# Optimization experiments

Hardware: AMD Instinct MI355X
Metric: run time of the kernel (lower is better)

The kernel has to match this reference:

```python
import jax, jax.numpy as jnp
import numpy as np

DIM = 1024   # model dim
H = 16       # query heads
KV = 2       # kv heads (GQA)
D = DIM // H # head_dim = 64
W = 256      # window_size
HW = W // 2  # half window = 128


def setup_inputs() -> dict:
    key = jax.random.key(0)
    ks = jax.random.split(key, 9)
    B, S = 2, 4096
    n = lambda k, shp, sc=1.0: jax.random.normal(k, shp, jnp.float32) * sc
    return {
        "x": n(ks[0], (B, S, DIM)),
        "Wq": n(ks[1], (DIM, H * D), 0.02), "bq": n(ks[2], (H * D,), 0.02),
        "Wk": n(ks[3], (DIM, KV * D), 0.02), "bk": n(ks[4], (KV * D,), 0.02),
        "Wv": n(ks[5], (DIM, KV * D), 0.02), "bv": n(ks[6], (KV * D,), 0.02),
        "Wo": n(ks[7], (DIM, DIM), 0.02), "bo": n(ks[8], (DIM,), 0.02),
    }


def reference(x, Wq, bq, Wk, bk, Wv, bv, Wo, bo):
    B, S, _ = x.shape
    # projections -> (b, h, s, d)
    q = (x @ Wq + bq).reshape(B, S, H, D).transpose(0, 2, 1, 3)
    k = (x @ Wk + bk).reshape(B, S, KV, D).transpose(0, 2, 1, 3)
    v = (x @ Wv + bv).reshape(B, S, KV, D).transpose(0, 2, 1, 3)
    # GQA: repeat_interleave kv heads to H heads
    rep = H // KV
    k = jnp.repeat(k, rep, axis=1)
    v = jnp.repeat(v, rep, axis=1)
    # zero-pad HW on each side of seq (faithful to F.pad in original):
    # padded boundary keys contribute raw score 0 inside the softmax.
    pad = ((0, 0), (0, 0), (HW, HW), (0, 0))
    pk = jnp.pad(k, pad)  # (b, h, S+W, d)
    pv = jnp.pad(v, pad)
    nblk = S // W
    # view padded keys as nblk+1 blocks of size W; each query block i uses
    # the 2W-span [i*W, i*W + 2W) of padded positions.
    pk = pk.reshape(B, H, nblk + 1, W, D)
    pv = pv.reshape(B, H, nblk + 1, W, D)
    kb = jnp.concatenate([pk[:, :, :-1], pk[:, :, 1:]], axis=3)  # (b,h,n,2W,d)
    vb = jnp.concatenate([pv[:, :, :-1], pv[:, :, 1:]], axis=3)
    qb = q.reshape(B, H, nblk, W, D)
    # NOTE: original training path has NO 1/sqrt(d) scaling.
    scores = jnp.einsum('bhntd,bhnud->bhntu', qb, kb)  # (b,h,n,W,2W)
    # query local t (global s=i*W+t) attends padded offsets u in [t, t+W),
    # i.e. global window [s-HW, s+HW-1] — exactly the original unfold.
    t = jnp.arange(W)[:, None]
    u = jnp.arange(2 * W)[None, :]
    win_mask = (u >= t) & (u < t + W)
    scores = jnp.where(win_mask, scores, -jnp.inf)
    probs = jax.nn.softmax(scores, axis=-1)
    out = jnp.einsum('bhntu,bhnud->bhntd', probs, vb)  # (b,h,n,W,d)
    out = out.reshape(B, H, S, D).transpose(0, 2, 1, 3).reshape(B, S, H * D)
    return out @ Wo + bo
```

## Files before the change

### kernel.cpp

```cpp
#include <hip/hip_runtime.h>
#include <hip/hip_bf16.h>


typedef __attribute__((ext_vector_type(4))) float f32x4;
typedef __attribute__((ext_vector_type(8))) short s16x8;
typedef __attribute__((ext_vector_type(4))) short s16x4;

#define SEQ    4096
#define NROWS  8192
#define QKV_N  1280

__device__ __forceinline__ unsigned short f2bf(float f) {
  union { float f; unsigned int u; } v; v.f = f;
  return (unsigned short)((v.u + 0x7FFFu + ((v.u >> 16) & 1u)) >> 16);
}

__device__ __forceinline__ void glds16(void* lds, const void* g) {
  void* gg = const_cast<void*>(g);
  __builtin_amdgcn_global_load_lds((__attribute__((address_space(1))) void*)gg,
                                   (__attribute__((address_space(3))) void*)lds,
                                   16, 0, 0);
}

__device__ __forceinline__ f32x4 mfma16(s16x8 a, s16x8 b, f32x4 c) {
  return __builtin_amdgcn_mfma_f32_16x16x32_bf16(a, b, c, 0, 0, 0);
}

__global__ void convert_x(const float* __restrict__ x,
                          unsigned short* __restrict__ xb, int n) {
  int idx = (blockIdx.x * 256 + threadIdx.x) * 4;
  if (idx >= n) return;
  f32x4 v = *(const f32x4*)(x + idx);
  s16x4 o;
  o[0] = (short)f2bf(v[0]); o[1] = (short)f2bf(v[1]);
  o[2] = (short)f2bf(v[2]); o[3] = (short)f2bf(v[3]);
  *(s16x4*)(xb + idx) = o;
}

__global__ void transpose_qkv(const float* __restrict__ Wq,
                              const float* __restrict__ Wk,
                              const float* __restrict__ Wv,
                              unsigned short* __restrict__ Wt) {
  __shared__ float tile[32][33];
  int k0 = blockIdx.x * 32, n0 = blockIdx.y * 32;
  const float* src; int ld, cn0;
  if (n0 < 1024)      { src = Wq; ld = 1024; cn0 = n0; }
  else if (n0 < 1152) { src = Wk; ld = 128;  cn0 = n0 - 1024; }
  else                { src = Wv; ld = 128;  cn0 = n0 - 1152; }
  int tx = threadIdx.x, ty = threadIdx.y;
  #pragma unroll
  for (int r = 0; r < 32; r += 8)
    tile[ty + r][tx] = src[(k0 + ty + r) * ld + cn0 + tx];
  __syncthreads();
  #pragma unroll
  for (int r = 0; r < 32; r += 8)
    Wt[(n0 + ty + r) * 1024 + k0 + tx] = f2bf(tile[tx][ty + r]);
}

__global__ void transpose_wo(const float* __restrict__ W,
                             unsigned short* __restrict__ Wt) {
  __shared__ float tile[32][33];
  int k0 = blockIdx.x * 32, n0 = blockIdx.y * 32;
  int tx = threadIdx.x, ty = threadIdx.y;
  #pragma unroll
  for (int r = 0; r < 32; r += 8)
    tile[ty + r][tx] = W[(k0 + ty + r) * 1024 + n0 + tx];
  __syncthreads();
  #pragma unroll
  for (int r = 0; r < 32; r += 8)
    Wt[(n0 + ty + r) * 1024 + k0 + tx] = f2bf(tile[tx][ty + r]);
}

template<bool BIAS3, bool OUT_F32>
__global__ __launch_bounds__(256)
void gemm_bt(const unsigned short* __restrict__ A,
             const unsigned short* __restrict__ Bt,
             void* __restrict__ Cv,
             const float* __restrict__ b0,
             const float* __restrict__ b1,
             const float* __restrict__ b2,
             int M, int N, int K) {
  __shared__ unsigned short la[128 * 32];
  __shared__ unsigned short lb[128 * 32];
  const int tid = threadIdx.x;
  const int lane = tid & 63;
  const int wv = tid >> 6;
  const int wr = wv >> 1, wc = wv & 1;
  const int l15 = lane & 15, lch = lane >> 4;
  const int row0 = blockIdx.x * 128;
  const int col0 = blockIdx.y * 128;

  f32x4 acc[4][4] = {};

  const int cc0 = tid, cc1 = 256 + tid;
  const unsigned short* a0 = A + (row0 + (cc0 >> 2)) * K + (cc0 & 3) * 8;
  const unsigned short* a1 = A + (row0 + (cc1 >> 2)) * K + (cc1 & 3) * 8;
  const unsigned short* bp0 = Bt + (col0 + (cc0 >> 2)) * K + (cc0 & 3) * 8;
  const unsigned short* bp1 = Bt + (col0 + (cc1 >> 2)) * K + (cc1 & 3) * 8;
  unsigned short* la0 = &la[cc0 * 8];
  unsigned short* la1 = &la[cc1 * 8];
  unsigned short* lb0 = &lb[cc0 * 8];
  unsigned short* lb1 = &lb[cc1 * 8];

  for (int k0 = 0; k0 < K; k0 += 32) {
    __syncthreads();
    glds16(la0, a0 + k0);
    glds16(la1, a1 + k0);
    glds16(lb0, bp0 + k0);
    glds16(lb1, bp1 + k0);
    asm volatile("s_waitcnt vmcnt(0)" ::: "memory");
    __syncthreads();

    s16x8 af[4], bfr[4];
    #pragma unroll
    for (int mi = 0; mi < 4; ++mi)
      af[mi] = *(const s16x8*)&la[(wr * 64 + mi * 16 + l15) * 32 + lch * 8];
    #pragma unroll
    for (int ni = 0; ni < 4; ++ni)
      bfr[ni] = *(const s16x8*)&lb[(wc * 64 + ni * 16 + l15) * 32 + lch * 8];
    #pragma unroll
    for (int mi = 0; mi < 4; ++mi)
      #pragma unroll
      for (int ni = 0; ni < 4; ++ni)
        acc[mi][ni] = mfma16(af[mi], bfr[ni], acc[mi][ni]);
  }

  #pragma unroll
  for (int mi = 0; mi < 4; ++mi) {
    #pragma unroll
    for (int ni = 0; ni < 4; ++ni) {
      int c = col0 + wc * 64 + ni * 16 + l15;
      float bias;
      if constexpr (BIAS3)
        bias = (c < 1024) ? b0[c] : (c < 1152) ? b1[c - 1024] : b2[c - 1152];
      else
        bias = b0[c];
      #pragma unroll
      for (int j = 0; j < 4; ++j) {
        int r = row0 + wr * 64 + mi * 16 + lch * 4 + j;
        float v = acc[mi][ni][j] + bias;
        if constexpr (OUT_F32) ((float*)Cv)[(long)r * N + c] = v;
        else ((unsigned short*)Cv)[(long)r * N + c] = f2bf(v);
      }
    }
  }
}

#define SPAN 320
#define VSTR 328

__global__ __launch_bounds__(256)
void attn_win(const unsigned short* __restrict__ qkv,
              unsigned short* __restrict__ aout) {
  __shared__ unsigned short Kl[SPAN * 64];
  __shared__ unsigned short Vt[64 * VSTR];
  __shared__ unsigned short Pl[4 * 16 * VSTR];

  const int tid = threadIdx.x;
  const int lane = tid & 63;
  const int w = tid >> 6;
  const int l15 = lane & 15, lch = lane >> 4;
  const int qt = blockIdx.x, h = blockIdx.y, b = blockIdx.z;
  const int kvh = h >> 3;
  const int qbase = qt * 64;
  const int kstart = qbase - 128;
  const int rowbase = b * SEQ;

  s16x8 qa0, qa1;
  {
    const unsigned short* src =
        qkv + (rowbase + qbase + w * 16 + l15) * QKV_N + h * 64 + lch * 8;
    qa0 = *(const s16x8*)src;
    qa1 = *(const s16x8*)(src + 32);
  }

  #pragma unroll
  for (int i = 0; i < 10; ++i) {
    int cc = i * 256 + tid;
    int row = cc >> 3;
    int col = (cc & 7) * 8;
    int key = kstart + row;
    s16x8 vk = {0, 0, 0, 0, 0, 0, 0, 0};
    s16x8 vv = {0, 0, 0, 0, 0, 0, 0, 0};
    if (key >= 0 && key < SEQ) {
      const unsigned short* base = qkv + (rowbase + key) * QKV_N;
      vk = *(const s16x8*)(base + 1024 + kvh * 64 + col);
      vv = *(const s16x8*)(base + 1152 + kvh * 64 + col);
    }
    int kb = (row * 128 + col * 2) ^ ((row & 7) << 4);
    *(s16x8*)((char*)Kl + kb) = vk;
    #pragma unroll
    for (int j = 0; j < 8; ++j)
      Vt[(col + j) * VSTR + row] = (unsigned short)vv[j];
  }
  __syncthreads();

  f32x4 sc[20];
  #pragma unroll
  for (int kt = 0; kt < 20; ++kt) {
    int key = kt * 16 + l15;
    int swz = (key & 7) << 4;
    s16x8 k0 = *(const s16x8*)((char*)Kl + ((key * 128 + lch * 16) ^ swz));
    s16x8 k1 = *(const s16x8*)((char*)Kl + ((key * 128 + 64 + lch * 16) ^ swz));
    f32x4 a = {0.f, 0.f, 0.f, 0.f};
    a = mfma16(qa0, k0, a);
    a = mfma16(qa1, k1, a);
    sc[kt] = a;
  }

  #pragma unroll
  for (int kt = 0; kt < 20; ++kt) {
    int u = kt * 16 + l15;
    int kpos = kstart + u;
    bool inr = (kpos >= 0) && (kpos < SEQ);
    #pragma unroll
    for (int j = 0; j < 4; ++j) {
      int tq = w * 16 + lch * 4 + j;
      float v = sc[kt][j];
      v = (u >= tq && u < tq + 256) ? (inr ? v : 0.0f) : -3.0e38f;
      sc[kt][j] = v;
    }
  }

  float inv[4];
  #pragma unroll
  for (int j = 0; j < 4; ++j) {
    float mx = sc[0][j];
    #pragma unroll
    for (int kt = 1; kt < 20; ++kt) mx = fmaxf(mx, sc[kt][j]);
    mx = fmaxf(mx, __shfl_xor(mx, 1, 64));
    mx = fmaxf(mx, __shfl_xor(mx, 2, 64));
    mx = fmaxf(mx, __shfl_xor(mx, 4, 64));
    mx = fmaxf(mx, __shfl_xor(mx, 8, 64));
    float sm = 0.f;
    #pragma unroll
    for (int kt = 0; kt < 20; ++kt) {
      float p = __expf(sc[kt][j] - mx);
      sc[kt][j] = p;
      sm += p;
    }
    sm += __shfl_xor(sm, 1, 64);
    sm += __shfl_xor(sm, 2, 64);
    sm += __shfl_xor(sm, 4, 64);
    sm += __shfl_xor(sm, 8, 64);
    inv[j] = 1.0f / sm;
  }

  unsigned short* Pw = Pl + w * 16 * VSTR;
  #pragma unroll
  for (int kt = 0; kt < 20; ++kt) {
    int u = kt * 16 + l15;
    int kpos = kstart + u;
    bool inr = (kpos >= 0) && (kpos < SEQ);
    #pragma unroll
    for (int j = 0; j < 4; ++j) {
      float p = inr ? sc[kt][j] * inv[j] : 0.0f;
      Pw[(lch * 4 + j) * VSTR + u] = f2bf(p);
    }
  }
  __syncthreads();

  f32x4 oa[4] = {};
  #pragma unroll
  for (int ks = 0; ks < 10; ++ks) {
    s16x8 pa = *(const s16x8*)&Pw[l15 * VSTR + ks * 32 + lch * 8];
    #pragma unroll
    for (int nt = 0; nt < 4; ++nt) {
      s16x8 bvf = *(const s16x8*)&Vt[(nt * 16 + l15) * VSTR + ks * 32 + lch * 8];
      oa[nt] = mfma16(pa, bvf, oa[nt]);
    }
  }

  #pragma unroll
  for (int nt = 0; nt < 4; ++nt)
    #pragma unroll
    for (int j = 0; j < 4; ++j) {
      int r = rowbase + qbase + w * 16 + lch * 4 + j;
      aout[(long)r * 1024 + h * 64 + nt * 16 + l15] = f2bf(oa[nt][j]);
    }
}

extern "C" void kernel_launch(void* const* d_in, const int* in_sizes, int n_in,
                              void* d_out, int out_size, void* d_ws, size_t ws_size,
                              hipStream_t stream) {
  const float* x  = (const float*)d_in[0];
  const float* Wq = (const float*)d_in[1];
  const float* bq = (const float*)d_in[2];
  const float* Wk = (const float*)d_in[3];
  const float* bk = (const float*)d_in[4];
  const float* Wv = (const float*)d_in[5];
  const float* bv = (const float*)d_in[6];
  const float* Wo = (const float*)d_in[7];
  const float* bo = (const float*)d_in[8];
  float* out = (float*)d_out;

  char* ws = (char*)d_ws;
  unsigned short* xb    = (unsigned short*)(ws);
  unsigned short* attno = (unsigned short*)(ws);
  unsigned short* wqkvt = (unsigned short*)(ws + 16777216);
  unsigned short* wot   = (unsigned short*)(ws + 19398656);
  unsigned short* qkv   = (unsigned short*)(ws + 21495808);

  convert_x<<<8192, 256, 0, stream>>>(x, xb, NROWS * 1024);
  transpose_qkv<<<dim3(32, 40), dim3(32, 8), 0, stream>>>(Wq, Wk, Wv, wqkvt);
  transpose_wo<<<dim3(32, 32), dim3(32, 8), 0, stream>>>(Wo, wot);

  gemm_bt<true, false><<<dim3(NROWS / 128, QKV_N / 128), 256, 0, stream>>>(
      xb, wqkvt, (void*)qkv, bq, bk, bv, NROWS, QKV_N, 1024);

  attn_win<<<dim3(64, 16, 2), 256, 0, stream>>>(qkv, attno);

  gemm_bt<false, true><<<dim3(NROWS / 128, 1024 / 128), 256, 0, stream>>>(
      attno, wot, (void*)out, bo, nullptr, nullptr, NROWS, 1024, 1024);
}
```

Baseline: 242.6 us.

## Share K/V tile across the 8 GQA heads and keep P in registers

Each attention block now covers one KV head with 8 warps, one per query head, so the K/V window is loaded into LDS once per group instead of once per query head. K is loaded straight into LDS with global_load_lds. The QK^T product is transposed so each lane holds the probabilities needed for the PV MFMA A-operand, which removes the LDS round trip for P and its barrier. V is stored with a permuted column order and a new stride to match that register layout. In exchange the grid is 8x smaller with 512-thread blocks and a serial loop over four 16-row query tiles, which cuts parallelism and raises register pressure.

New measurement: 255.8 us. 1.05x slower.

```diff
diff --git a/kernel.cpp b/kernel.cpp
--- a/kernel.cpp
+++ b/kernel.cpp
@@ -13,6 +13,12 @@
 __device__ __forceinline__ unsigned short f2bf(float f) {
   union { float f; unsigned int u; } v; v.f = f;
   return (unsigned short)((v.u + 0x7FFFu + ((v.u >> 16) & 1u)) >> 16);
+}
+
+__device__ __forceinline__ unsigned int pk2(float lo, float hi) {
+  __hip_bfloat162 h = __float22bfloat162_rn(make_float2(lo, hi));
+  union { __hip_bfloat162 h; unsigned int u; } c; c.h = h;
+  return c.u;
 }
 
 __device__ __forceinline__ void glds16(void* lds, const void* g) {
@@ -147,137 +153,140 @@
 }
 
 #define SPAN 320
-#define VSTR 328
-
-__global__ __launch_bounds__(256)
+#define VSTR 332
+
+__global__ __launch_bounds__(512, 2)
 void attn_win(const unsigned short* __restrict__ qkv,
               unsigned short* __restrict__ aout) {
   __shared__ unsigned short Kl[SPAN * 64];
   __shared__ unsigned short Vt[64 * VSTR];
-  __shared__ unsigned short Pl[4 * 16 * VSTR];
 
   const int tid = threadIdx.x;
   const int lane = tid & 63;
   const int w = tid >> 6;
   const int l15 = lane & 15, lch = lane >> 4;
-  const int qt = blockIdx.x, h = blockIdx.y, b = blockIdx.z;
-  const int kvh = h >> 3;
+  const int qt = blockIdx.x, kvh = blockIdx.y, b = blockIdx.z;
+  const int h = kvh * 8 + w;
   const int qbase = qt * 64;
   const int kstart = qbase - 128;
   const int rowbase = b * SEQ;
 
-  s16x8 qa0, qa1;
-  {
-    const unsigned short* src =
-        qkv + (rowbase + qbase + w * 16 + l15) * QKV_N + h * 64 + lch * 8;
-    qa0 = *(const s16x8*)src;
-    qa1 = *(const s16x8*)(src + 32);
-  }
-
-  #pragma unroll
-  for (int i = 0; i < 10; ++i) {
-    int cc = i * 256 + tid;
-    int row = cc >> 3;
-    int col = (cc & 7) * 8;
-    int key = kstart + row;
-    s16x8 vk = {0, 0, 0, 0, 0, 0, 0, 0};
-    s16x8 vv = {0, 0, 0, 0, 0, 0, 0, 0};
-    if (key >= 0 && key < SEQ) {
-      const unsigned short* base = qkv + (rowbase + key) * QKV_N;
-      vk = *(const s16x8*)(base + 1024 + kvh * 64 + col);
-      vv = *(const s16x8*)(base + 1152 + kvh * 64 + col);
+  s16x8 vv[5];
+  #pragma unroll
+  for (int i = 0; i < 5; ++i) {
+    int cc = i * 512 + tid;
+    int u = cc >> 3;
+    int c8 = cc & 7;
+    int key = kstart + u;
+    key = key < 0 ? 0 : (key > SEQ - 1 ? SEQ - 1 : key);
+    vv[i] = *(const s16x8*)(qkv + (long)(rowbase + key) * QKV_N + 1152 + kvh * 64 + c8 * 8);
+  }
+  #pragma unroll
+  for (int i = 0; i < 5; ++i) {
+    int cc = i * 512 + tid;
+    int u = cc >> 3;
+    int c16s = (cc & 7) ^ (u & 7);
+    int key = kstart + u;
+    key = key < 0 ? 0 : (key > SEQ - 1 ? SEQ - 1 : key);
+    glds16((char*)Kl + cc * 16,
+           qkv + (long)(rowbase + key) * QKV_N + 1024 + kvh * 64 + c16s * 8);
+  }
+  #pragma unroll
+  for (int i = 0; i < 5; ++i) {
+    int cc = i * 512 + tid;
+    int u = cc >> 3;
+    int c8 = cc & 7;
+    int su = (u & ~31) | (((u >> 2) & 3) << 3) | (((u >> 4) & 1) << 2) | (u & 3);
+    #pragma unroll
+    for (int j = 0; j < 8; ++j)
+      Vt[(c8 * 8 + j) * VSTR + su] = (unsigned short)vv[i][j];
+  }
+  asm volatile("s_waitcnt vmcnt(0)" ::: "memory");
+  __syncthreads();
+
+  for (int mt = 0; mt < 4; ++mt) {
+    const unsigned short* qp =
+        qkv + (long)(rowbase + qbase + mt * 16 + l15) * QKV_N + h * 64 + lch * 8;
+    s16x8 qf0 = *(const s16x8*)qp;
+    s16x8 qf1 = *(const s16x8*)(qp + 32);
+
+    f32x4 sc[20];
+    #pragma unroll
+    for (int kt = 0; kt < 20; ++kt) {
+      int key = kt * 16 + l15;
+      int swz = (key & 7) << 4;
+      const char* kb = (const char*)Kl + key * 128;
+      s16x8 k0 = *(const s16x8*)(kb + ((lch * 16) ^ swz));
+      s16x8 k1 = *(const s16x8*)(kb + ((64 + lch * 16) ^ swz));
+      f32x4 a = {0.f, 0.f, 0.f, 0.f};
+      a = mfma16(k0, qf0, a);
+      a = mfma16(k1, qf1, a);
+      sc[kt] = a;
     }
-    int kb = (row * 128 + col * 2) ^ ((row & 7) << 4);
-    *(s16x8*)((char*)Kl + kb) = vk;
-    #pragma unroll
-    for (int j = 0; j < 8; ++j)
-      Vt[(col + j) * VSTR + row] = (unsigned short)vv[j];
-  }
-  __syncthreads();
-
-  f32x4 sc[20];
-  #pragma unroll
-  for (int kt = 0; kt < 20; ++kt) {
-    int key = kt * 16 + l15;
-    int swz = (key & 7) << 4;
-    s16x8 k0 = *(const s16x8*)((char*)Kl + ((key * 128 + lch * 16) ^ swz));
-    s16x8 k1 = *(const s16x8*)((char*)Kl + ((key * 128 + 64 + lch * 16) ^ swz));
-    f32x4 a = {0.f, 0.f, 0.f, 0.f};
-    a = mfma16(qa0, k0, a);
-    a = mfma16(qa1, k1, a);
-    sc[kt] = a;
-  }
-
-  #pragma unroll
-  for (int kt = 0; kt < 20; ++kt) {
-    int u = kt * 16 + l15;
-    int kpos = kstart + u;
-    bool inr = (kpos >= 0) && (kpos < SEQ);
-    #pragma unroll
-    for (int j = 0; j < 4; ++j) {
-      int tq = w * 16 + lch * 4 + j;
-      float v = sc[kt][j];
-      v = (u >= tq && u < tq + 256) ? (inr ? v : 0.0f) : -3.0e38f;
-      sc[kt][j] = v;
+
+    int tq = mt * 16 + l15;
+    float mx = -3.0e38f;
+    #pragma unroll
+    for (int kt = 0; kt < 20; ++kt)
+      #pragma unroll
+      for (int j = 0; j < 4; ++j) {
+        int u = kt * 16 + lch * 4 + j;
+        int kpos = kstart + u;
+        bool win = (u >= tq) && (u < tq + 256);
+        bool inr = (kpos >= 0) && (kpos < SEQ);
+        float v = win ? (inr ? sc[kt][j] : 0.0f) : -3.0e38f;
+        sc[kt][j] = v;
+        mx = fmaxf(mx, v);
+      }
+    mx = fmaxf(mx, __shfl_xor(mx, 16));
+    mx = fmaxf(mx, __shfl_xor(mx, 32));
+    float sm = 0.f;
+    #pragma unroll
+    for (int kt = 0; kt < 20; ++kt)
+      #pragma unroll
+      for (int j = 0; j < 4; ++j) {
+        float p = __expf(sc[kt][j] - mx);
+        sc[kt][j] = p;
+        sm += p;
+      }
+    sm += __shfl_xor(sm, 16);
+    sm += __shfl_xor(sm, 32);
+    float inv = 1.0f / sm;
+    #pragma unroll
+    for (int kt = 0; kt < 20; ++kt)
+      #pragma unroll
+      for (int j = 0; j < 4; ++j) {
+        int kpos = kstart + kt * 16 + lch * 4 + j;
+        bool inr = (kpos >= 0) && (kpos < SEQ);
+        sc[kt][j] = inr ? sc[kt][j] * inv : 0.0f;
+      }
+
+    f32x4 oa[4] = {};
+    #pragma unroll
+    for (int c = 0; c < 10; ++c) {
+      union { unsigned int wd[4]; s16x8 v; } af;
+      af.wd[0] = pk2(sc[2 * c][0], sc[2 * c][1]);
+      af.wd[1] = pk2(sc[2 * c][2], sc[2 * c][3]);
+      af.wd[2] = pk2(sc[2 * c + 1][0], sc[2 * c + 1][1]);
+      af.wd[3] = pk2(sc[2 * c + 1][2], sc[2 * c + 1][3]);
+      #pragma unroll
+      for (int nt = 0; nt < 4; ++nt) {
+        const unsigned short* vp = &Vt[(nt * 16 + l15) * VSTR + c * 32 + lch * 8];
+        union { unsigned long long q[2]; s16x8 v; } bf_;
+        bf_.q[0] = *(const unsigned long long*)vp;
+        bf_.q[1] = *(const unsigned long long*)(vp + 4);
+        oa[nt] = mfma16(af.v, bf_.v, oa[nt]);
+      }
     }
-  }
-
-  float inv[4];
-  #pragma unroll
-  for (int j = 0; j < 4; ++j) {
-    float mx = sc[0][j];
-    #pragma unroll
-    for (int kt = 1; kt < 20; ++kt) mx = fmaxf(mx, sc[kt][j]);
-    mx = fmaxf(mx, __shfl_xor(mx, 1, 64));
-    mx = fmaxf(mx, __shfl_xor(mx, 2, 64));
-    mx = fmaxf(mx, __shfl_xor(mx, 4, 64));
-    mx = fmaxf(mx, __shfl_xor(mx, 8, 64));
-    float sm = 0.f;
-    #pragma unroll
-    for (int kt = 0; kt < 20; ++kt) {
-      float p = __expf(sc[kt][j] - mx);
-      sc[kt][j] = p;
-      sm += p;
-    }
-    sm += __shfl_xor(sm, 1, 64);
-    sm += __shfl_xor(sm, 2, 64);
-    sm += __shfl_xor(sm, 4, 64);
-    sm += __shfl_xor(sm, 8, 64);
-    inv[j] = 1.0f / sm;
-  }
-
-  unsigned short* Pw = Pl + w * 16 * VSTR;
-  #pragma unroll
-  for (int kt = 0; kt < 20; ++kt) {
-    int u = kt * 16 + l15;
-    int kpos = kstart + u;
-    bool inr = (kpos >= 0) && (kpos < SEQ);
-    #pragma unroll
-    for (int j = 0; j < 4; ++j) {
-      float p = inr ? sc[kt][j] * inv[j] : 0.0f;
-      Pw[(lch * 4 + j) * VSTR + u] = f2bf(p);
-    }
-  }
-  __syncthreads();
-
-  f32x4 oa[4] = {};
-  #pragma unroll
-  for (int ks = 0; ks < 10; ++ks) {
-    s16x8 pa = *(const s16x8*)&Pw[l15 * VSTR + ks * 32 + lch * 8];
-    #pragma unroll
-    for (int nt = 0; nt < 4; ++nt) {
-      s16x8 bvf = *(const s16x8*)&Vt[(nt * 16 + l15) * VSTR + ks * 32 + lch * 8];
-      oa[nt] = mfma16(pa, bvf, oa[nt]);
-    }
-  }
-
-  #pragma unroll
-  for (int nt = 0; nt < 4; ++nt)
-    #pragma unroll
-    for (int j = 0; j < 4; ++j) {
-      int r = rowbase + qbase + w * 16 + lch * 4 + j;
-      aout[(long)r * 1024 + h * 64 + nt * 16 + l15] = f2bf(oa[nt][j]);
-    }
+
+    #pragma unroll
+    for (int nt = 0; nt < 4; ++nt)
+      #pragma unroll
+      for (int j = 0; j < 4; ++j) {
+        long r = rowbase + qbase + mt * 16 + lch * 4 + j;
+        aout[r * 1024 + h * 64 + nt * 16 + l15] = f2bf(oa[nt][j]);
+      }
+  }
 }
 
 extern "C" void kernel_launch(void* const* d_in, const int* in_sizes, int n_in,
@@ -308,7 +317,7 @@
   gemm_bt<true, false><<<dim3(NROWS / 128, QKV_N / 128), 256, 0, stream>>>(
       xb, wqkvt, (void*)qkv, bq, bk, bv, NROWS, QKV_N, 1024);
 
-  attn_win<<<dim3(64, 16, 2), 256, 0, stream>>>(qkv, attno);
+  attn_win<<<dim3(64, 2, 2), 512, 0, stream>>>(qkv, attno);
 
   gemm_bt<false, true><<<dim3(NROWS / 128, 1024 / 128), 256, 0, stream>>>(
       attno, wot, (void*)out, bo, nullptr, nullptr, NROWS, 1024, 1024);
```
